# Kernel optimization log

Measured on AMD Instinct MI355X. Metric: run time of the kernel, lower is better.

The kernel has to match this reference:

```python
import jax, jax.numpy as jnp
import numpy as np

VOCAB = 32000   # vocab size
EDIM = 1024     # embedding dim
HDIM = 1024     # encoder hidden dim (fhid dim)
NACTS = 2       # ACTS = {'push': 0, 'pop': 1}
NCLASSES = 3
L = 256         # len_total
B = 128         # bsz
PAD = 0         # padding_idx
PUSH, POP = 0, 1


def setup_inputs() -> dict:
    key = jax.random.key(0)
    ks = jax.random.split(key, 10)

    def mk_seq(kt, kl):
        tok = jax.random.randint(kt, (L, B), 1, VOCAB)          # non-pad tokens
        lens = jax.random.randint(kl, (B,), L // 2, L - 1)      # ragged lengths
        t = jnp.arange(L)[:, None]
        # first lens+1 positions non-pad (so lens = L - n_pad - 1 as in the module)
        return jnp.where(t < lens[None, :] + 1, tok, PAD)

    seq1 = mk_seq(ks[0], ks[1])
    seq2 = mk_seq(ks[2], ks[3])

    def w(k, shp):
        return (jax.random.normal(k, shp, jnp.float32) * 0.02)

    return {
        "seq1": seq1, "seq2": seq2,
        "emb": w(ks[4], (VOCAB, EDIM)),
        "W_top": w(ks[5], (EDIM, HDIM)), "b_top": jnp.zeros((HDIM,), jnp.float32),
        "W_act": w(ks[6], (EDIM, NACTS)), "b_act": jnp.zeros((NACTS,), jnp.float32),
        "W1": w(ks[7], (4 * HDIM, HDIM)), "b1": jnp.zeros((HDIM,), jnp.float32),
        "W2": w(ks[8], (HDIM, NCLASSES)), "b2": jnp.zeros((NCLASSES,), jnp.float32),
    }


def _encode(seq, emb, W_top, b_top, W_act, b_act):
    # stub stack-encoder: time dim 2L-1 (one shift + one reduce step per token)
    seq_ext = jnp.concatenate([seq, seq[:-1]], axis=0)          # [2L-1, B]
    x = emb[seq_ext]                                            # [2L-1, B, E]
    top = jnp.tanh(jnp.einsum('tbe,eh->tbh', x, W_top) + b_top) # [2L-1, B, H]
    act = jax.nn.softmax(jnp.einsum('tbe,ea->tba', x, W_act) + b_act, axis=-1)
    return top, act


def _ragged_stats(act, Ts, bsz):
    # masked equivalents of the per-sample python loops over acts[:T, b, :]
    Tmax = act.shape[0]
    mask = (jnp.arange(Tmax)[:, None] < Ts[None, :]).astype(act.dtype)  # [2L-1, B]
    Tf = Ts.astype(act.dtype)
    push, pop = act[:, :, PUSH], act[:, :, POP]
    sum_push = (push * mask).sum(axis=0) / Tf                   # [B]
    sum_pop = ((pop * mask).sum(axis=0) + 1.0) / Tf             # [B]
    diff = jnp.sqrt((((push - pop) ** 2) * mask).sum(axis=0)) / Tf  # [B]
    dis = jnp.linalg.norm(sum_push - sum_pop) / bsz             # scalar
    return dis, diff.sum() / bsz


def reference(seq1, seq2, emb, W_top, b_top, W_act, b_act, W1, b1, W2, b2):
    bsz = seq1.shape[1]
    top1, act1 = _encode(seq1, emb, W_top, b_top, W_act, b_act)
    top2, act2 = _encode(seq2, emb, W_top, b_top, W_act, b_act)

    lens1 = seq1.shape[0] - (seq1 == PAD).sum(axis=0) - 1
    lens2 = seq2.shape[0] - (seq2 == PAD).sum(axis=0) - 1
    Ts1 = 2 * lens1 - 1
    Ts2 = 2 * lens2 - 1

    barange = jnp.arange(bsz)
    fhid1 = top1[Ts1 - 1, barange]                              # [B, H] ragged gather
    fhid2 = top2[Ts2 - 1, barange]

    u = jnp.concatenate([fhid1, fhid2, jnp.abs(fhid1 - fhid2), fhid1 * fhid2], axis=-1)
    res_clf = jax.nn.relu(u @ W1 + b1) @ W2 + b2                # [B, nclasses]

    dis1, diff1 = _ragged_stats(act1, Ts1, bsz)
    dis2, diff2 = _ragged_stats(act2, Ts2, bsz)
    return (res_clf, dis1, dis2, diff1, diff2)
```

## Files before the change

### kernel.cpp

```cpp
#include <hip/hip_runtime.h>
#include <math.h>

#define LL 256
#define BB 128
#define EDIM 1024
#define HDIM 1024
#define VOCAB 32000

#define WS_EACT   0
#define WS_DELTA  64000
#define WS_DIFFB  64256
#define WS_TOKF   64512
#define WS_FHID   64768
#define WS_BIG    326912

__device__ __forceinline__ void fma4(float4& acc, float s, const float4& w) {
  acc.x = fmaf(s, w.x, acc.x); acc.y = fmaf(s, w.y, acc.y);
  acc.z = fmaf(s, w.z, acc.z); acc.w = fmaf(s, w.w, acc.w);
}

extern "C" __global__ __launch_bounds__(256)
void k_eact(const float* __restrict__ emb, const float* __restrict__ Wact,
            float* __restrict__ Eact, float* __restrict__ out) {
  if (blockIdx.x == 0 && threadIdx.x < 96)
    ((float4*)out)[threadIdx.x] = make_float4(0.f, 0.f, 0.f, 0.f);
  int lane = threadIdx.x & 63;
  int wave = threadIdx.x >> 6;
  int v = blockIdx.x * 4 + wave;
  const float4* row = (const float4*)(emb + (size_t)v * EDIM);
  const float4* w4 = (const float4*)Wact;
  float a0 = 0.f, a1 = 0.f;
#pragma unroll
  for (int it = 0; it < 4; ++it) {
    int i = lane + it * 64;
    float4 x = row[i];
    float4 wa = w4[2 * i];
    float4 wb = w4[2 * i + 1];
    a0 = fmaf(x.x, wa.x, a0); a0 = fmaf(x.y, wa.z, a0);
    a0 = fmaf(x.z, wb.x, a0); a0 = fmaf(x.w, wb.z, a0);
    a1 = fmaf(x.x, wa.y, a1); a1 = fmaf(x.y, wa.w, a1);
    a1 = fmaf(x.z, wb.y, a1); a1 = fmaf(x.w, wb.w, a1);
  }
#pragma unroll
  for (int off = 32; off; off >>= 1) {
    a0 += __shfl_down(a0, off, 64);
    a1 += __shfl_down(a1, off, 64);
  }
  if (lane == 0) { Eact[2 * v] = a0; Eact[2 * v + 1] = a1; }
}

extern "C" __global__ __launch_bounds__(256)
void k_stats(const int* __restrict__ seq1, const int* __restrict__ seq2,
             const float* __restrict__ Eact, const float* __restrict__ b_act,
             float* __restrict__ delta, float* __restrict__ diffb,
             int* __restrict__ tokf) {
  int bx = blockIdx.x;
  int s = bx >> 7, b = bx & 127;
  const int* seq = s ? seq2 : seq1;
  int tid = threadIdx.x;
  __shared__ int col[LL];
  __shared__ int redi[256];
  __shared__ float redf[256];
  col[tid] = seq[tid * BB + b];
  __syncthreads();
  redi[tid] = (col[tid] == 0) ? 1 : 0;
  __syncthreads();
  for (int off = 128; off; off >>= 1) {
    if (tid < off) redi[tid] += redi[tid + off];
    __syncthreads();
  }
  int lens = LL - redi[0] - 1;
  int Ts = 2 * lens - 1;
  float ba = b_act[0] - b_act[1];
  float sp = 0.f, spp = 0.f, sq = 0.f;
  for (int t = tid; t < Ts; t += 256) {
    int tok = (t < LL) ? col[t] : col[t - LL];
    float2 e = ((const float2*)Eact)[tok];
    float d = e.x - e.y + ba;
    float p0 = 1.0f / (1.0f + expf(-d));
    float p1 = 1.0f - p0;
    sp += p0; spp += p1;
    float dd = p0 - p1;
    sq = fmaf(dd, dd, sq);
  }
  redf[tid] = sp; __syncthreads();
  for (int off = 128; off; off >>= 1) { if (tid < off) redf[tid] += redf[tid + off]; __syncthreads(); }
  float tsp = redf[0]; __syncthreads();
  redf[tid] = spp; __syncthreads();
  for (int off = 128; off; off >>= 1) { if (tid < off) redf[tid] += redf[tid + off]; __syncthreads(); }
  float tspp = redf[0]; __syncthreads();
  redf[tid] = sq; __syncthreads();
  for (int off = 128; off; off >>= 1) { if (tid < off) redf[tid] += redf[tid + off]; __syncthreads(); }
  float tsq = redf[0];
  if (tid == 0) {
    float Tf = (float)Ts;
    delta[bx] = (tsp - tspp - 1.0f) / Tf;
    diffb[bx] = sqrtf(tsq) / Tf;
    int tt = Ts - 1;
    tokf[bx] = (tt < LL) ? col[tt] : col[tt - LL];
  }
}

extern "C" __global__ __launch_bounds__(256)
void k_final(const float* __restrict__ delta, const float* __restrict__ diffb,
             float* __restrict__ out) {
  __shared__ float red[256];
  int tid = threadIdx.x;
  for (int s = 0; s < 2; ++s) {
    float v = 0.f, w = 0.f;
    if (tid < BB) { float d = delta[s * BB + tid]; v = d * d; w = diffb[s * BB + tid]; }
    red[tid] = v; __syncthreads();
    for (int off = 128; off; off >>= 1) { if (tid < off) red[tid] += red[tid + off]; __syncthreads(); }
    if (tid == 0) out[384 + s] = sqrtf(red[0]) / (float)BB;
    __syncthreads();
    red[tid] = w; __syncthreads();
    for (int off = 128; off; off >>= 1) { if (tid < off) red[tid] += red[tid + off]; __syncthreads(); }
    if (tid == 0) out[386 + s] = red[0] / (float)BB;
    __syncthreads();
  }
}

extern "C" __global__ __launch_bounds__(256)
void k_fpart(const float* __restrict__ emb, const float* __restrict__ Wtop,
             const int* __restrict__ tokf, float* __restrict__ fpart, int nch) {
  int cb = blockIdx.x, rb = blockIdx.y, ks = blockIdx.z;
  int tid = threadIdx.x;
  int cg = tid & 15, rgr = tid >> 4;
  int c0 = cb * 64 + cg * 4;
  int kbase = ks * nch * 64;
  __shared__ float ash[128 * 64];
  __shared__ int stok[128];
  if (tid < 128) stok[tid] = tokf[rb * 128 + tid];
  float4 acc[8];
#pragma unroll
  for (int r = 0; r < 8; ++r) acc[r] = make_float4(0.f, 0.f, 0.f, 0.f);
  for (int ch = 0; ch < nch; ++ch) {
    int kg = kbase + ch * 64;
    __syncthreads();
    for (int idx = tid; idx < 128 * 16; idx += 256) {
      int r = idx >> 4, q = idx & 15;
      ((float4*)ash)[idx] = ((const float4*)(emb + (size_t)stok[r] * EDIM + kg))[q];
    }
    __syncthreads();
    const float* Wp = Wtop + (size_t)kg * HDIM + c0;
    float4 w[4];
#pragma unroll
    for (int j = 0; j < 4; ++j) w[j] = *(const float4*)(Wp + (size_t)j * HDIM);
#pragma unroll
    for (int kk = 0; kk < 64; kk += 4) {
      float4 wn[4];
      if (kk + 4 < 64) {
#pragma unroll
        for (int j = 0; j < 4; ++j) wn[j] = *(const float4*)(Wp + (size_t)(kk + 4 + j) * HDIM);
      }
#pragma unroll
      for (int r = 0; r < 8; ++r) {
        float4 a = *(const float4*)&ash[(rgr * 8 + r) * 64 + kk];
        fma4(acc[r], a.x, w[0]); fma4(acc[r], a.y, w[1]);
        fma4(acc[r], a.z, w[2]); fma4(acc[r], a.w, w[3]);
      }
#pragma unroll
      for (int j = 0; j < 4; ++j) w[j] = wn[j];
    }
  }
  float* dst = fpart + ((size_t)ks * 256 + rb * 128 + rgr * 8) * HDIM + c0;
#pragma unroll
  for (int r = 0; r < 8; ++r)
    *(float4*)(dst + (size_t)r * HDIM) = acc[r];
}

extern "C" __global__ __launch_bounds__(256)
void k_ftanh(const float* __restrict__ fpart, const float* __restrict__ btop,
             float* __restrict__ fhid, int nksf) {
  int g = blockIdx.x * 256 + threadIdx.x;
  float4 s = ((const float4*)fpart)[g];
  for (int k = 1; k < nksf; ++k) {
    float4 p = ((const float4*)fpart)[(size_t)k * 65536 + g];
    s.x += p.x; s.y += p.y; s.z += p.z; s.w += p.w;
  }
  float4 b = ((const float4*)btop)[g & 255];
  float4 o;
  o.x = tanhf(s.x + b.x); o.y = tanhf(s.y + b.y);
  o.z = tanhf(s.z + b.z); o.w = tanhf(s.w + b.w);
  ((float4*)fhid)[g] = o;
}

extern "C" __global__ __launch_bounds__(256)
void k_part(const float* __restrict__ fhid, const float* __restrict__ W1,
            float* __restrict__ part, int nch) {
  int cb = blockIdx.x, ksb = blockIdx.y;
  int tid = threadIdx.x;
  int cg = tid & 15, rgr = tid >> 4;
  int c0 = cb * 64 + cg * 4;
  int kbase = ksb * nch * 64;
  __shared__ float ush[128 * 64];
  float4 acc[8];
#pragma unroll
  for (int r = 0; r < 8; ++r) acc[r] = make_float4(0.f, 0.f, 0.f, 0.f);
  const float4* f4 = (const float4*)fhid;
  for (int ch = 0; ch < nch; ++ch) {
    int kg = kbase + ch * 64;
    int seg = kg >> 10;
    int fb4 = (kg & 1023) >> 2;
    __syncthreads();
    for (int idx = tid; idx < 128 * 16; idx += 256) {
      int r = idx >> 4, q = idx & 15;
      float4 u;
      if (seg == 0) {
        u = f4[r * 256 + fb4 + q];
      } else if (seg == 1) {
        u = f4[(128 + r) * 256 + fb4 + q];
      } else {
        float4 f1 = f4[r * 256 + fb4 + q];
        float4 f2 = f4[(128 + r) * 256 + fb4 + q];
        if (seg == 2)
          u = make_float4(fabsf(f1.x - f2.x), fabsf(f1.y - f2.y),
                          fabsf(f1.z - f2.z), fabsf(f1.w - f2.w));
        else
          u = make_float4(f1.x * f2.x, f1.y * f2.y, f1.z * f2.z, f1.w * f2.w);
      }
      ((float4*)ush)[idx] = u;
    }
    __syncthreads();
    const float* Wp = W1 + (size_t)kg * HDIM + c0;
    float4 w[4];
#pragma unroll
    for (int j = 0; j < 4; ++j) w[j] = *(const float4*)(Wp + (size_t)j * HDIM);
#pragma unroll
    for (int kk = 0; kk < 64; kk += 4) {
      float4 wn[4];
      if (kk + 4 < 64) {
#pragma unroll
        for (int j = 0; j < 4; ++j) wn[j] = *(const float4*)(Wp + (size_t)(kk + 4 + j) * HDIM);
      }
#pragma unroll
      for (int r = 0; r < 8; ++r) {
        float4 a = *(const float4*)&ush[(rgr * 8 + r) * 64 + kk];
        fma4(acc[r], a.x, w[0]); fma4(acc[r], a.y, w[1]);
        fma4(acc[r], a.z, w[2]); fma4(acc[r], a.w, w[3]);
      }
#pragma unroll
      for (int j = 0; j < 4; ++j) w[j] = wn[j];
    }
  }
  float* dst = part + ((size_t)ksb * 128 + rgr * 8) * HDIM + c0;
#pragma unroll
  for (int r = 0; r < 8; ++r)
    *(float4*)(dst + (size_t)r * HDIM) = acc[r];
}

extern "C" __global__ __launch_bounds__(256)
void k_clf(const float* __restrict__ part, const float* __restrict__ b1,
           const float* __restrict__ W2, const float* __restrict__ b2,
           float* __restrict__ out, int nks) {
  int b = blockIdx.x, kq = blockIdx.y;
  int tid = threadIdx.x;
  int k = kq * 256 + tid;
  float p = b1[k];
  for (int ks = 0; ks < nks; ++ks)
    p += part[((size_t)ks * 128 + b) * HDIM + k];
  p = fmaxf(p, 0.f);
  float a0 = p * W2[k * 3 + 0];
  float a1 = p * W2[k * 3 + 1];
  float a2 = p * W2[k * 3 + 2];
  __shared__ float red[768];
  red[tid] = a0; red[256 + tid] = a1; red[512 + tid] = a2;
  __syncthreads();
  for (int off = 128; off; off >>= 1) {
    if (tid < off) {
      red[tid] += red[tid + off];
      red[256 + tid] += red[256 + tid + off];
      red[512 + tid] += red[512 + tid + off];
    }
    __syncthreads();
  }
  if (tid == 0) {
    float e0 = red[0], e1 = red[256], e2 = red[512];
    if (kq == 0) { e0 += b2[0]; e1 += b2[1]; e2 += b2[2]; }
    atomicAdd(out + b * 3 + 0, e0);
    atomicAdd(out + b * 3 + 1, e1);
    atomicAdd(out + b * 3 + 2, e2);
  }
}

extern "C" void kernel_launch(void* const* d_in, const int* in_sizes, int n_in,
                              void* d_out, int out_size, void* d_ws, size_t ws_size,
                              hipStream_t stream) {
  const int*   seq1  = (const int*)  d_in[0];
  const int*   seq2  = (const int*)  d_in[1];
  const float* emb   = (const float*)d_in[2];
  const float* W_top = (const float*)d_in[3];
  const float* b_top = (const float*)d_in[4];
  const float* W_act = (const float*)d_in[5];
  const float* b_act = (const float*)d_in[6];
  const float* W1    = (const float*)d_in[7];
  const float* b1    = (const float*)d_in[8];
  const float* W2    = (const float*)d_in[9];
  const float* b2    = (const float*)d_in[10];
  float* out = (float*)d_out;
  float* ws  = (float*)d_ws;

  bool big = ws_size >= (size_t)20 * 1024 * 1024;
  int nks  = big ? 32 : 16;
  int nch  = 64 / nks;
  int nksf = big ? 16 : 8;
  int nchf = 16 / nksf;

  float* Eact  = ws + WS_EACT;
  float* delta = ws + WS_DELTA;
  float* diffb = ws + WS_DIFFB;
  int*   tokf  = (int*)(ws + WS_TOKF);
  float* fhid  = ws + WS_FHID;
  float* bigb  = ws + WS_BIG;

  hipLaunchKernelGGL(k_eact,  dim3(VOCAB / 4),       dim3(256), 0, stream, emb, W_act, Eact, out);
  hipLaunchKernelGGL(k_stats, dim3(256),             dim3(256), 0, stream, seq1, seq2, Eact, b_act, delta, diffb, tokf);
  hipLaunchKernelGGL(k_final, dim3(1),               dim3(256), 0, stream, delta, diffb, out);
  hipLaunchKernelGGL(k_fpart, dim3(16, 2, nksf),     dim3(256), 0, stream, emb, W_top, tokf, bigb, nchf);
  hipLaunchKernelGGL(k_ftanh, dim3(256),             dim3(256), 0, stream, bigb, b_top, fhid, nksf);
  hipLaunchKernelGGL(k_part,  dim3(16, nks),         dim3(256), 0, stream, fhid, W1, bigb, nch);
  hipLaunchKernelGGL(k_clf,   dim3(128, 4),          dim3(256), 0, stream, bigb, b1, W2, b2, out, nks);
}
```

Before: 280.7 us.

## Merge independent stages into shared launches and pad LDS tiles

```diff
diff --git a/kernel.cpp b/kernel.cpp
--- a/kernel.cpp
+++ b/kernel.cpp
@@ -7,142 +7,225 @@
 #define HDIM 1024
 #define VOCAB 32000
 
+#define NKSF 16
+#define NKS  32
+
 #define WS_EACT   0
 #define WS_DELTA  64000
 #define WS_DIFFB  64256
 #define WS_TOKF   64512
-#define WS_FHID   64768
-#define WS_BIG    326912
-
-__device__ __forceinline__ void fma4(float4& acc, float s, const float4& w) {
-  acc.x = fmaf(s, w.x, acc.x); acc.y = fmaf(s, w.y, acc.y);
-  acc.z = fmaf(s, w.z, acc.z); acc.w = fmaf(s, w.w, acc.w);
-}
-
-extern "C" __global__ __launch_bounds__(256)
-void k_eact(const float* __restrict__ emb, const float* __restrict__ Wact,
-            float* __restrict__ Eact, float* __restrict__ out) {
-  if (blockIdx.x == 0 && threadIdx.x < 96)
-    ((float4*)out)[threadIdx.x] = make_float4(0.f, 0.f, 0.f, 0.f);
-  int lane = threadIdx.x & 63;
-  int wave = threadIdx.x >> 6;
-  int v = blockIdx.x * 4 + wave;
-  const float4* row = (const float4*)(emb + (size_t)v * EDIM);
-  const float4* w4 = (const float4*)Wact;
-  float a0 = 0.f, a1 = 0.f;
-#pragma unroll
-  for (int it = 0; it < 4; ++it) {
-    int i = lane + it * 64;
-    float4 x = row[i];
-    float4 wa = w4[2 * i];
-    float4 wb = w4[2 * i + 1];
-    a0 = fmaf(x.x, wa.x, a0); a0 = fmaf(x.y, wa.z, a0);
-    a0 = fmaf(x.z, wb.x, a0); a0 = fmaf(x.w, wb.z, a0);
-    a1 = fmaf(x.x, wa.y, a1); a1 = fmaf(x.y, wa.w, a1);
-    a1 = fmaf(x.z, wb.y, a1); a1 = fmaf(x.w, wb.w, a1);
-  }
-#pragma unroll
-  for (int off = 32; off; off >>= 1) {
-    a0 += __shfl_down(a0, off, 64);
-    a1 += __shfl_down(a1, off, 64);
-  }
-  if (lane == 0) { Eact[2 * v] = a0; Eact[2 * v + 1] = a1; }
-}
-
-extern "C" __global__ __launch_bounds__(256)
-void k_stats(const int* __restrict__ seq1, const int* __restrict__ seq2,
-             const float* __restrict__ Eact, const float* __restrict__ b_act,
-             float* __restrict__ delta, float* __restrict__ diffb,
-             int* __restrict__ tokf) {
-  int bx = blockIdx.x;
+#define WS_TS     64768
+#define WS_FHID   65024
+#define WS_BIG    327168
+
+#define APAD 68
+
+__device__ __forceinline__ void fma4(float4& a, float s, const float4& w) {
+  a.x = fmaf(s, w.x, a.x); a.y = fmaf(s, w.y, a.y);
+  a.z = fmaf(s, w.z, a.z); a.w = fmaf(s, w.w, a.w);
+}
+
+extern "C" __global__ __launch_bounds__(256)
+void k_prep(const int* __restrict__ seq1, const int* __restrict__ seq2,
+            int* __restrict__ tokf, int* __restrict__ Tsv, float* __restrict__ out) {
+  int bx = blockIdx.x, tid = threadIdx.x;
+  if (bx == 0 && tid < 96) ((float4*)out)[tid] = make_float4(0.f, 0.f, 0.f, 0.f);
   int s = bx >> 7, b = bx & 127;
   const int* seq = s ? seq2 : seq1;
-  int tid = threadIdx.x;
   __shared__ int col[LL];
-  __shared__ int redi[256];
-  __shared__ float redf[256];
-  col[tid] = seq[tid * BB + b];
-  __syncthreads();
-  redi[tid] = (col[tid] == 0) ? 1 : 0;
+  __shared__ int red[256];
+  int v = seq[tid * BB + b];
+  col[tid] = v;
+  red[tid] = (v == 0) ? 1 : 0;
   __syncthreads();
   for (int off = 128; off; off >>= 1) {
-    if (tid < off) redi[tid] += redi[tid + off];
-    __syncthreads();
-  }
-  int lens = LL - redi[0] - 1;
-  int Ts = 2 * lens - 1;
-  float ba = b_act[0] - b_act[1];
-  float sp = 0.f, spp = 0.f, sq = 0.f;
-  for (int t = tid; t < Ts; t += 256) {
-    int tok = (t < LL) ? col[t] : col[t - LL];
-    float2 e = ((const float2*)Eact)[tok];
-    float d = e.x - e.y + ba;
-    float p0 = 1.0f / (1.0f + expf(-d));
-    float p1 = 1.0f - p0;
-    sp += p0; spp += p1;
-    float dd = p0 - p1;
-    sq = fmaf(dd, dd, sq);
-  }
-  redf[tid] = sp; __syncthreads();
-  for (int off = 128; off; off >>= 1) { if (tid < off) redf[tid] += redf[tid + off]; __syncthreads(); }
-  float tsp = redf[0]; __syncthreads();
-  redf[tid] = spp; __syncthreads();
-  for (int off = 128; off; off >>= 1) { if (tid < off) redf[tid] += redf[tid + off]; __syncthreads(); }
-  float tspp = redf[0]; __syncthreads();
-  redf[tid] = sq; __syncthreads();
-  for (int off = 128; off; off >>= 1) { if (tid < off) redf[tid] += redf[tid + off]; __syncthreads(); }
-  float tsq = redf[0];
+    if (tid < off) red[tid] += red[tid + off];
+    __syncthreads();
+  }
   if (tid == 0) {
-    float Tf = (float)Ts;
-    delta[bx] = (tsp - tspp - 1.0f) / Tf;
-    diffb[bx] = sqrtf(tsq) / Tf;
+    int lens = LL - red[0] - 1;
+    int Ts = 2 * lens - 1;
+    Tsv[bx] = Ts;
     int tt = Ts - 1;
     tokf[bx] = (tt < LL) ? col[tt] : col[tt - LL];
   }
 }
 
 extern "C" __global__ __launch_bounds__(256)
-void k_final(const float* __restrict__ delta, const float* __restrict__ diffb,
-             float* __restrict__ out) {
-  __shared__ float red[256];
-  int tid = threadIdx.x;
-  for (int s = 0; s < 2; ++s) {
-    float v = 0.f, w = 0.f;
-    if (tid < BB) { float d = delta[s * BB + tid]; v = d * d; w = diffb[s * BB + tid]; }
-    red[tid] = v; __syncthreads();
-    for (int off = 128; off; off >>= 1) { if (tid < off) red[tid] += red[tid + off]; __syncthreads(); }
-    if (tid == 0) out[384 + s] = sqrtf(red[0]) / (float)BB;
-    __syncthreads();
-    red[tid] = w; __syncthreads();
-    for (int off = 128; off; off >>= 1) { if (tid < off) red[tid] += red[tid + off]; __syncthreads(); }
-    if (tid == 0) out[386 + s] = red[0] / (float)BB;
-    __syncthreads();
-  }
-}
-
-extern "C" __global__ __launch_bounds__(256)
-void k_fpart(const float* __restrict__ emb, const float* __restrict__ Wtop,
-             const int* __restrict__ tokf, float* __restrict__ fpart, int nch) {
-  int cb = blockIdx.x, rb = blockIdx.y, ks = blockIdx.z;
-  int tid = threadIdx.x;
+void k_fh_eact(const float* __restrict__ emb, const float* __restrict__ Wtop,
+               const float* __restrict__ Wact, const int* __restrict__ tokf,
+               float* __restrict__ fpart, float* __restrict__ Eact) {
+  __shared__ float ash[128 * APAD];
+  __shared__ int stok[128];
+  int blk = blockIdx.x, tid = threadIdx.x;
+  if (blk >= 512) {
+    int lane = tid & 63, wave = tid >> 6;
+    int v = (blk - 512) * 4 + wave;
+    const float4* row = (const float4*)(emb + (size_t)v * EDIM);
+    const float4* w4 = (const float4*)Wact;
+    float a0 = 0.f, a1 = 0.f;
+#pragma unroll
+    for (int it = 0; it < 4; ++it) {
+      int i = lane + it * 64;
+      float4 x = row[i];
+      float4 wa = w4[2 * i];
+      float4 wb = w4[2 * i + 1];
+      a0 = fmaf(x.x, wa.x, a0); a0 = fmaf(x.y, wa.z, a0);
+      a0 = fmaf(x.z, wb.x, a0); a0 = fmaf(x.w, wb.z, a0);
+      a1 = fmaf(x.x, wa.y, a1); a1 = fmaf(x.y, wa.w, a1);
+      a1 = fmaf(x.z, wb.y, a1); a1 = fmaf(x.w, wb.w, a1);
+    }
+#pragma unroll
+    for (int off = 32; off; off >>= 1) {
+      a0 += __shfl_down(a0, off, 64);
+      a1 += __shfl_down(a1, off, 64);
+    }
+    if (lane == 0) { Eact[2 * v] = a0; Eact[2 * v + 1] = a1; }
+    return;
+  }
+  int ks = blk >> 5, rb = (blk >> 4) & 1, cb = blk & 15;
   int cg = tid & 15, rgr = tid >> 4;
   int c0 = cb * 64 + cg * 4;
-  int kbase = ks * nch * 64;
-  __shared__ float ash[128 * 64];
-  __shared__ int stok[128];
+  int kg = ks * 64;
   if (tid < 128) stok[tid] = tokf[rb * 128 + tid];
+  __syncthreads();
+  for (int idx = tid; idx < 128 * 16; idx += 256) {
+    int r = idx >> 4, q = idx & 15;
+    *(float4*)&ash[r * APAD + q * 4] =
+        ((const float4*)(emb + (size_t)stok[r] * EDIM + kg))[q];
+  }
+  __syncthreads();
+  const float* Wp = Wtop + (size_t)kg * HDIM + c0;
   float4 acc[8];
 #pragma unroll
   for (int r = 0; r < 8; ++r) acc[r] = make_float4(0.f, 0.f, 0.f, 0.f);
-  for (int ch = 0; ch < nch; ++ch) {
+  float4 w[4];
+#pragma unroll
+  for (int j = 0; j < 4; ++j) w[j] = *(const float4*)(Wp + (size_t)j * HDIM);
+#pragma unroll
+  for (int kk = 0; kk < 64; kk += 4) {
+    float4 wn[4];
+    if (kk + 4 < 64) {
+#pragma unroll
+      for (int j = 0; j < 4; ++j) wn[j] = *(const float4*)(Wp + (size_t)(kk + 4 + j) * HDIM);
+    }
+#pragma unroll
+    for (int r = 0; r < 8; ++r) {
+      float4 a = *(const float4*)&ash[(rgr * 8 + r) * APAD + kk];
+      fma4(acc[r], a.x, w[0]); fma4(acc[r], a.y, w[1]);
+      fma4(acc[r], a.z, w[2]); fma4(acc[r], a.w, w[3]);
+    }
+#pragma unroll
+    for (int j = 0; j < 4; ++j) w[j] = wn[j];
+  }
+  float* dst = fpart + ((size_t)ks * 256 + rb * 128 + rgr * 8) * HDIM + c0;
+#pragma unroll
+  for (int r = 0; r < 8; ++r)
+    *(float4*)(dst + (size_t)r * HDIM) = acc[r];
+}
+
+extern "C" __global__ __launch_bounds__(256)
+void k_ftanh(const float* __restrict__ fpart, const float* __restrict__ btop,
+             float* __restrict__ fhid) {
+  int g = blockIdx.x * 256 + threadIdx.x;
+  float4 s = ((const float4*)fpart)[g];
+#pragma unroll
+  for (int k = 1; k < NKSF; ++k) {
+    float4 p = ((const float4*)fpart)[(size_t)k * 65536 + g];
+    s.x += p.x; s.y += p.y; s.z += p.z; s.w += p.w;
+  }
+  float4 b = ((const float4*)btop)[g & 255];
+  ((float4*)fhid)[g] = make_float4(tanhf(s.x + b.x), tanhf(s.y + b.y),
+                                   tanhf(s.z + b.z), tanhf(s.w + b.w));
+}
+
+extern "C" __global__ __launch_bounds__(256)
+void k_part_stats(const float* __restrict__ fhid, const float* __restrict__ W1,
+                  const int* __restrict__ seq1, const int* __restrict__ seq2,
+                  const float* __restrict__ Eact, const float* __restrict__ b_act,
+                  const int* __restrict__ Tsv,
+                  float* __restrict__ part, float* __restrict__ delta,
+                  float* __restrict__ diffb) {
+  __shared__ float ush[128 * APAD];
+  int blk = blockIdx.x, tid = threadIdx.x;
+  if (blk >= 512) {
+    int sb = blk - 512;
+    int s = sb >> 7, b = sb & 127;
+    const int* seq = s ? seq2 : seq1;
+    int* col = (int*)ush;
+    float* redf = ush + 256;
+    col[tid] = seq[tid * BB + b];
+    __syncthreads();
+    int Ts = Tsv[sb];
+    float ba = b_act[0] - b_act[1];
+    float sp = 0.f, sq = 0.f;
+    for (int t = tid; t < Ts; t += 256) {
+      int tok = (t < LL) ? col[t] : col[t - LL];
+      float2 e = ((const float2*)Eact)[tok];
+      float d = e.x - e.y + ba;
+      float p0 = 1.0f / (1.0f + expf(-d));
+      float dd = 2.f * p0 - 1.f;
+      sp += dd;
+      sq = fmaf(dd, dd, sq);
+    }
+    redf[tid] = sp; __syncthreads();
+    for (int off = 128; off; off >>= 1) { if (tid < off) redf[tid] += redf[tid + off]; __syncthreads(); }
+    float tsp = redf[0]; __syncthreads();
+    redf[tid] = sq; __syncthreads();
+    for (int off = 128; off; off >>= 1) { if (tid < off) redf[tid] += redf[tid + off]; __syncthreads(); }
+    if (tid == 0) {
+      float Tf = (float)Ts;
+      delta[sb] = (tsp - 1.0f) / Tf;
+      diffb[sb] = sqrtf(redf[0]) / Tf;
+    }
+    return;
+  }
+  int ksb = blk >> 4, cb = blk & 15;
+  int cg = tid & 15, rgr = tid >> 4;
+  int c0 = cb * 64 + cg * 4;
+  int kbase = ksb * 128;
+  int seg = kbase >> 10;
+  const float4* f4 = (const float4*)fhid;
+  float4 acc[8];
+#pragma unroll
+  for (int r = 0; r < 8; ++r) acc[r] = make_float4(0.f, 0.f, 0.f, 0.f);
+  float4 sreg[8];
+#define GATHER(ch)                                                        \
+  {                                                                       \
+    int fb4 = ((kbase + (ch) * 64) & 1023) >> 2;                          \
+    _Pragma("unroll")                                                     \
+    for (int j = 0; j < 8; ++j) {                                         \
+      int idx = tid + j * 256;                                            \
+      int r = idx >> 4, q = idx & 15;                                     \
+      float4 u;                                                           \
+      if (seg == 0) u = f4[r * 256 + fb4 + q];                            \
+      else if (seg == 1) u = f4[(128 + r) * 256 + fb4 + q];               \
+      else {                                                              \
+        float4 f1 = f4[r * 256 + fb4 + q];                                \
+        float4 f2 = f4[(128 + r) * 256 + fb4 + q];                        \
+        if (seg == 2)                                                     \
+          u = make_float4(fabsf(f1.x - f2.x), fabsf(f1.y - f2.y),         \
+                          fabsf(f1.z - f2.z), fabsf(f1.w - f2.w));        \
+        else                                                              \
+          u = make_float4(f1.x * f2.x, f1.y * f2.y, f1.z * f2.z, f1.w * f2.w); \
+      }                                                                   \
+      sreg[j] = u;                                                        \
+    }                                                                     \
+  }
+  GATHER(0)
+#pragma unroll
+  for (int ch = 0; ch < 2; ++ch) {
+    __syncthreads();
+#pragma unroll
+    for (int j = 0; j < 8; ++j) {
+      int idx = tid + j * 256;
+      int r = idx >> 4, q = idx & 15;
+      *(float4*)&ush[r * APAD + q * 4] = sreg[j];
+    }
+    __syncthreads();
+    if (ch == 0) GATHER(1)
     int kg = kbase + ch * 64;
-    __syncthreads();
-    for (int idx = tid; idx < 128 * 16; idx += 256) {
-      int r = idx >> 4, q = idx & 15;
-      ((float4*)ash)[idx] = ((const float4*)(emb + (size_t)stok[r] * EDIM + kg))[q];
-    }
-    __syncthreads();
-    const float* Wp = Wtop + (size_t)kg * HDIM + c0;
+    const float* Wp = W1 + (size_t)kg * HDIM + c0;
     float4 w[4];
 #pragma unroll
     for (int j = 0; j < 4; ++j) w[j] = *(const float4*)(Wp + (size_t)j * HDIM);
@@ -155,7 +238,7 @@
       }
 #pragma unroll
       for (int r = 0; r < 8; ++r) {
-        float4 a = *(const float4*)&ash[(rgr * 8 + r) * 64 + kk];
+        float4 a = *(const float4*)&ush[(rgr * 8 + r) * APAD + kk];
         fma4(acc[r], a.x, w[0]); fma4(acc[r], a.y, w[1]);
         fma4(acc[r], a.z, w[2]); fma4(acc[r], a.w, w[3]);
       }
@@ -163,107 +246,45 @@
       for (int j = 0; j < 4; ++j) w[j] = wn[j];
     }
   }
-  float* dst = fpart + ((size_t)ks * 256 + rb * 128 + rgr * 8) * HDIM + c0;
+#undef GATHER
+  float* dst = part + ((size_t)ksb * 128 + rgr * 8) * HDIM + c0;
 #pragma unroll
   for (int r = 0; r < 8; ++r)
     *(float4*)(dst + (size_t)r * HDIM) = acc[r];
 }
 
 extern "C" __global__ __launch_bounds__(256)
-void k_ftanh(const float* __restrict__ fpart, const float* __restrict__ btop,
-             float* __restrict__ fhid, int nksf) {
-  int g = blockIdx.x * 256 + threadIdx.x;
-  float4 s = ((const float4*)fpart)[g];
-  for (int k = 1; k < nksf; ++k) {
-    float4 p = ((const float4*)fpart)[(size_t)k * 65536 + g];
-    s.x += p.x; s.y += p.y; s.z += p.z; s.w += p.w;
-  }
-  float4 b = ((const float4*)btop)[g & 255];
-  float4 o;
-  o.x = tanhf(s.x + b.x); o.y = tanhf(s.y + b.y);
-  o.z = tanhf(s.z + b.z); o.w = tanhf(s.w + b.w);
-  ((float4*)fhid)[g] = o;
-}
-
-extern "C" __global__ __launch_bounds__(256)
-void k_part(const float* __restrict__ fhid, const float* __restrict__ W1,
-            float* __restrict__ part, int nch) {
-  int cb = blockIdx.x, ksb = blockIdx.y;
-  int tid = threadIdx.x;
-  int cg = tid & 15, rgr = tid >> 4;
-  int c0 = cb * 64 + cg * 4;
-  int kbase = ksb * nch * 64;
-  __shared__ float ush[128 * 64];
-  float4 acc[8];
-#pragma unroll
-  for (int r = 0; r < 8; ++r) acc[r] = make_float4(0.f, 0.f, 0.f, 0.f);
-  const float4* f4 = (const float4*)fhid;
-  for (int ch = 0; ch < nch; ++ch) {
-    int kg = kbase + ch * 64;
-    int seg = kg >> 10;
-    int fb4 = (kg & 1023) >> 2;
-    __syncthreads();
-    for (int idx = tid; idx < 128 * 16; idx += 256) {
-      int r = idx >> 4, q = idx & 15;
-      float4 u;
-      if (seg == 0) {
-        u = f4[r * 256 + fb4 + q];
-      } else if (seg == 1) {
-        u = f4[(128 + r) * 256 + fb4 + q];
-      } else {
-        float4 f1 = f4[r * 256 + fb4 + q];
-        float4 f2 = f4[(128 + r) * 256 + fb4 + q];
-        if (seg == 2)
-          u = make_float4(fabsf(f1.x - f2.x), fabsf(f1.y - f2.y),
-                          fabsf(f1.z - f2.z), fabsf(f1.w - f2.w));
-        else
-          u = make_float4(f1.x * f2.x, f1.y * f2.y, f1.z * f2.z, f1.w * f2.w);
-      }
-      ((float4*)ush)[idx] = u;
-    }
-    __syncthreads();
-    const float* Wp = W1 + (size_t)kg * HDIM + c0;
-    float4 w[4];
-#pragma unroll
-    for (int j = 0; j < 4; ++j) w[j] = *(const float4*)(Wp + (size_t)j * HDIM);
-#pragma unroll
-    for (int kk = 0; kk < 64; kk += 4) {
-      float4 wn[4];
-      if (kk + 4 < 64) {
-#pragma unroll
-        for (int j = 0; j < 4; ++j) wn[j] = *(const float4*)(Wp + (size_t)(kk + 4 + j) * HDIM);
-      }
-#pragma unroll
-      for (int r = 0; r < 8; ++r) {
-        float4 a = *(const float4*)&ush[(rgr * 8 + r) * 64 + kk];
-        fma4(acc[r], a.x, w[0]); fma4(acc[r], a.y, w[1]);
-        fma4(acc[r], a.z, w[2]); fma4(acc[r], a.w, w[3]);
-      }
-#pragma unroll
-      for (int j = 0; j < 4; ++j) w[j] = wn[j];
-    }
-  }
-  float* dst = part + ((size_t)ksb * 128 + rgr * 8) * HDIM + c0;
-#pragma unroll
-  for (int r = 0; r < 8; ++r)
-    *(float4*)(dst + (size_t)r * HDIM) = acc[r];
-}
-
-extern "C" __global__ __launch_bounds__(256)
-void k_clf(const float* __restrict__ part, const float* __restrict__ b1,
-           const float* __restrict__ W2, const float* __restrict__ b2,
-           float* __restrict__ out, int nks) {
-  int b = blockIdx.x, kq = blockIdx.y;
-  int tid = threadIdx.x;
+void k_clf_final(const float* __restrict__ part, const float* __restrict__ b1,
+                 const float* __restrict__ W2, const float* __restrict__ b2,
+                 const float* __restrict__ delta, const float* __restrict__ diffb,
+                 float* __restrict__ out) {
+  int blk = blockIdx.x, tid = threadIdx.x;
+  __shared__ float red[768];
+  if (blk == 512) {
+    for (int s = 0; s < 2; ++s) {
+      float v = 0.f, w = 0.f;
+      if (tid < BB) { float d = delta[s * BB + tid]; v = d * d; w = diffb[s * BB + tid]; }
+      red[tid] = v; __syncthreads();
+      for (int off = 128; off; off >>= 1) { if (tid < off) red[tid] += red[tid + off]; __syncthreads(); }
+      if (tid == 0) out[384 + s] = sqrtf(red[0]) / (float)BB;
+      __syncthreads();
+      red[tid] = w; __syncthreads();
+      for (int off = 128; off; off >>= 1) { if (tid < off) red[tid] += red[tid + off]; __syncthreads(); }
+      if (tid == 0) out[386 + s] = red[0] / (float)BB;
+      __syncthreads();
+    }
+    return;
+  }
+  int b = blk >> 2, kq = blk & 3;
   int k = kq * 256 + tid;
   float p = b1[k];
-  for (int ks = 0; ks < nks; ++ks)
+#pragma unroll
+  for (int ks = 0; ks < NKS; ++ks)
     p += part[((size_t)ks * 128 + b) * HDIM + k];
   p = fmaxf(p, 0.f);
   float a0 = p * W2[k * 3 + 0];
   float a1 = p * W2[k * 3 + 1];
   float a2 = p * W2[k * 3 + 2];
-  __shared__ float red[768];
   red[tid] = a0; red[256 + tid] = a1; red[512 + tid] = a2;
   __syncthreads();
   for (int off = 128; off; off >>= 1) {
@@ -300,24 +321,17 @@
   float* out = (float*)d_out;
   float* ws  = (float*)d_ws;
 
-  bool big = ws_size >= (size_t)20 * 1024 * 1024;
-  int nks  = big ? 32 : 16;
-  int nch  = 64 / nks;
-  int nksf = big ? 16 : 8;
-  int nchf = 16 / nksf;
-
   float* Eact  = ws + WS_EACT;
   float* delta = ws + WS_DELTA;
   float* diffb = ws + WS_DIFFB;
   int*   tokf  = (int*)(ws + WS_TOKF);
+  int*   Tsv   = (int*)(ws + WS_TS);
   float* fhid  = ws + WS_FHID;
   float* bigb  = ws + WS_BIG;
 
-  hipLaunchKernelGGL(k_eact,  dim3(VOCAB / 4),       dim3(256), 0, stream, emb, W_act, Eact, out);
-  hipLaunchKernelGGL(k_stats, dim3(256),             dim3(256), 0, stream, seq1, seq2, Eact, b_act, delta, diffb, tokf);
-  hipLaunchKernelGGL(k_final, dim3(1),               dim3(256), 0, stream, delta, diffb, out);
-  hipLaunchKernelGGL(k_fpart, dim3(16, 2, nksf),     dim3(256), 0, stream, emb, W_top, tokf, bigb, nchf);
-  hipLaunchKernelGGL(k_ftanh, dim3(256),             dim3(256), 0, stream, bigb, b_top, fhid, nksf);
-  hipLaunchKernelGGL(k_part,  dim3(16, nks),         dim3(256), 0, stream, fhid, W1, bigb, nch);
-  hipLaunchKernelGGL(k_clf,   dim3(128, 4),          dim3(256), 0, stream, bigb, b1, W2, b2, out, nks);
-}
+  hipLaunchKernelGGL(k_prep,       dim3(256),        dim3(256), 0, stream, seq1, seq2, tokf, Tsv, out);
+  hipLaunchKernelGGL(k_fh_eact,    dim3(512 + 8000), dim3(256), 0, stream, emb, W_top, W_act, tokf, bigb, Eact);
+  hipLaunchKernelGGL(k_ftanh,      dim3(256),        dim3(256), 0, stream, bigb, b_top, fhid);
+  hipLaunchKernelGGL(k_part_stats, dim3(768),        dim3(256), 0, stream, fhid, W1, seq1, seq2, Eact, b_act, Tsv, bigb, delta, diffb);
+  hipLaunchKernelGGL(k_clf_final,  dim3(513),        dim3(256), 0, stream, bigb, b1, W2, b2, delta, diffb, out);
+}
```

Result: faster. 271.9 us (-3.1%).
